# Kernel tuning notes

Hardware: AMD Instinct MI355X
Metric: run time of the kernel (lower is better)

Reference implementation:

```python
import jax, jax.numpy as jnp
import numpy as np
from jax import lax

B, L, D, N, NL, P = 4, 2048, 256, 16, 2, 200
CNN_CH = [(1, 128), (128, 256), (256, 256), (256, 256)]

def _pe(length, dim):
    pos = np.arange(length)[:, None].astype(np.float32)
    div = np.exp(np.arange(0, dim, 2).astype(np.float32) * (-np.log(10000.0) / dim))
    pe = np.zeros((length, dim), np.float32)
    pe[:, 0::2] = np.sin(pos * div)
    pe[:, 1::2] = np.cos(pos * div)
    return jnp.asarray(pe)

def _ln(x, g, b):
    m = x.mean(-1, keepdims=True)
    v = x.var(-1, keepdims=True)
    return (x - m) * lax.rsqrt(v + 1e-5) * g + b

def _ssm(u, A_log, dt_w, dt_b, B_w, C_w, Dp):
    # selective scan: h_t = a_t*h_{t-1} + b_t ; y_t = <h_t, C_t> + D*u_t
    dt = jax.nn.softplus(u @ dt_w + dt_b)                      # [B,L,d]
    A = -jnp.exp(A_log)                                        # [d,n]
    a = jnp.exp(dt[..., None] * A)                             # [B,L,d,n]
    Bu = jnp.einsum('bld,dn->bln', u, B_w)
    bv = dt[..., None] * Bu[:, :, None, :] * u[..., None]      # [B,L,d,n]
    C = jnp.einsum('bld,dn->bln', u, C_w)
    def step(h, ab):
        at, bt = ab
        h = at * h + bt
        return h, h
    _, hs = lax.scan(step, jnp.zeros_like(a[:, 0]), (jnp.moveaxis(a, 1, 0), jnp.moveaxis(bv, 1, 0)))
    hs = jnp.moveaxis(hs, 0, 1)                                # [B,L,d,n]
    return jnp.einsum('bldn,bln->bld', hs, C) + u * Dp

def _bimamba(x, g, bt, in_w, in_b, A_log, dt_w, dt_b, B_w, C_w, Dp, out_w, out_b):
    h = _ln(x, g, bt)
    u, z = jnp.split(h @ in_w + in_b, 2, axis=-1)
    u = jax.nn.silu(u)
    yf = _ssm(u, A_log[0], dt_w[0], dt_b[0], B_w[0], C_w[0], Dp[0])
    yb = jnp.flip(_ssm(jnp.flip(u, 1), A_log[1], dt_w[1], dt_b[1], B_w[1], C_w[1], Dp[1]), 1)
    return ((yf + yb) * jax.nn.silu(z)) @ out_w + out_b

def _forward(x, pairs, emb_w, emb_b, conv0_w, conv0_b, bn0_g, bn0_b, conv1_w, conv1_b, bn1_g, bn1_b, conv2_w, conv2_b, bn2_g, bn2_b, conv3_w, conv3_b, bn3_g, bn3_b, fp_w, fp_b, mb_norm_g, mb_norm_b, mb_in_w, mb_in_b, mb_A_log, mb_dt_w, mb_dt_b, mb_B_w, mb_C_w, mb_D, mb_out_w, mb_out_b, me_w1, me_b1, me_w2, me_b2, mew, ep_w, ep_b, epi_w1, epi_b1, epi_w2, epi_b2, epi_w3, epi_b3, out_w1, out_b1, out_w2, out_b2):
    x_embed = x[..., None] * emb_w + emb_b                     # snp_embedding: Linear(1,D)
    h = x[:, None, :]                                          # [B,1,L]
    for cw, cb, g, b in ((conv0_w, conv0_b, bn0_g, bn0_b), (conv1_w, conv1_b, bn1_g, bn1_b), (conv2_w, conv2_b, bn2_g, bn2_b), (conv3_w, conv3_b, bn3_g, bn3_b)):
        h = lax.conv_general_dilated(h, cw, (1,), [(1, 1)], dimension_numbers=('NCH', 'OIH', 'NCH')) + cb[None, :, None]
        h = jax.nn.relu(g[None, :, None] * h + b[None, :, None])  # eval-mode BatchNorm (running stats)
    x_cnn = jnp.transpose(h, (0, 2, 1))                        # [B,L,C]
    xm = x_embed + (x_cnn @ fp_w + fp_b) + _pe(L, D)           # combine + sinusoidal PE
    for l in range(NL):
        xm = xm + _bimamba(xm, mb_norm_g[l], mb_norm_b[l], mb_in_w[l], mb_in_b[l], mb_A_log[l], mb_dt_w[l], mb_dt_b[l], mb_B_w[l], mb_C_w[l], mb_D[l], mb_out_w[l], mb_out_b[l])
    x_final = xm
    x_main = jax.nn.relu(x @ me_w1 + me_b1) @ me_w2 + me_b2    # main_effect MLP
    main_weights = jax.nn.sigmoid(mew)
    # batched pairwise epistasis scoring (replaces the Python pair loop)
    fi = x_final[:, pairs[:, 0], :]                            # [B,P,D]
    fj = x_final[:, pairs[:, 1], :]
    scores = jax.nn.sigmoid(jnp.concatenate([fi, fj], -1) @ ep_w + ep_b)[..., 0].mean(0)  # [P]
    top_scores, top_idx = lax.top_k(scores, P)
    top_pairs = pairs[top_idx]
    x_flat = jnp.concatenate([x_cnn.mean(1), x_final.mean(1), x_main], -1)  # [B, C+D+16]
    e = jax.nn.relu(x_flat @ epi_w1 + epi_b1)
    e = jax.nn.relu(e @ epi_w2 + epi_b2)
    e = e @ epi_w3 + epi_b3
    pred = jax.nn.sigmoid(jax.nn.relu(e @ out_w1 + out_b1) @ out_w2 + out_b2)
    return pred, main_weights, top_pairs, top_scores

def setup_inputs():
    kit = iter(jax.random.split(jax.random.key(0), 64))
    def nrm(shape, s=0.02):
        return jax.random.normal(next(kit), shape, jnp.float32) * s
    z = lambda *s: jnp.zeros(s, jnp.float32)
    o = lambda *s: jnp.ones(s, jnp.float32)
    inp = {}
    inp['x'] = jax.random.normal(next(kit), (B, L), jnp.float32)
    i = jax.random.randint(next(kit), (P,), 0, L)
    off = jax.random.randint(next(kit), (P,), 1, L)
    inp['pairs'] = jnp.stack([i, (i + off) % L], axis=1).astype(jnp.int32)
    inp['emb_w'] = nrm((D,), 0.1); inp['emb_b'] = z(D)
    for li, (ci, co) in enumerate(CNN_CH):
        inp['conv%d_w' % li] = nrm((co, ci, 3), 0.1)
        inp['conv%d_b' % li] = z(co)
        inp['bn%d_g' % li] = o(co)
        inp['bn%d_b' % li] = z(co)
    inp['fp_w'] = nrm((CNN_CH[-1][1], D)); inp['fp_b'] = z(D)
    inp['mb_norm_g'] = o(NL, D); inp['mb_norm_b'] = z(NL, D)
    inp['mb_in_w'] = nrm((NL, D, 2 * D)); inp['mb_in_b'] = z(NL, 2 * D)
    inp['mb_A_log'] = jnp.log(jnp.broadcast_to(jnp.arange(1, N + 1, dtype=jnp.float32), (NL, 2, D, N)))
    inp['mb_dt_w'] = nrm((NL, 2, D, D)); inp['mb_dt_b'] = jnp.full((NL, 2, D), -3.0, jnp.float32)
    inp['mb_B_w'] = nrm((NL, 2, D, N)); inp['mb_C_w'] = nrm((NL, 2, D, N))
    inp['mb_D'] = o(NL, 2, D)
    inp['mb_out_w'] = nrm((NL, D, D)); inp['mb_out_b'] = z(NL, D)
    inp['me_w1'] = nrm((L, D)); inp['me_b1'] = z(D)
    inp['me_w2'] = nrm((D, 16)); inp['me_b2'] = z(16)
    inp['mew'] = jax.random.normal(next(kit), (L,), jnp.float32)
    inp['ep_w'] = nrm((2 * D, 1)); inp['ep_b'] = z(1)
    inp['epi_w1'] = nrm((CNN_CH[-1][1] + D + 16, 128)); inp['epi_b1'] = z(128)
    inp['epi_w2'] = nrm((128, 64)); inp['epi_b2'] = z(64)
    inp['epi_w3'] = nrm((64, 32)); inp['epi_b3'] = z(32)
    inp['out_w1'] = nrm((32, 16)); inp['out_b1'] = z(16)
    inp['out_w2'] = nrm((16, 1)); inp['out_b2'] = z(1)
    return inp

def reference(x, pairs, emb_w, emb_b, conv0_w, conv0_b, bn0_g, bn0_b, conv1_w, conv1_b, bn1_g, bn1_b, conv2_w, conv2_b, bn2_g, bn2_b, conv3_w, conv3_b, bn3_g, bn3_b, fp_w, fp_b, mb_norm_g, mb_norm_b, mb_in_w, mb_in_b, mb_A_log, mb_dt_w, mb_dt_b, mb_B_w, mb_C_w, mb_D, mb_out_w, mb_out_b, me_w1, me_b1, me_w2, me_b2, mew, ep_w, ep_b, epi_w1, epi_b1, epi_w2, epi_b2, epi_w3, epi_b3, out_w1, out_b1, out_w2, out_b2):
    return _forward(x, pairs, emb_w, emb_b, conv0_w, conv0_b, bn0_g, bn0_b, conv1_w, conv1_b, bn1_g, bn1_b, conv2_w, conv2_b, bn2_g, bn2_b, conv3_w, conv3_b, bn3_g, bn3_b, fp_w, fp_b, mb_norm_g, mb_norm_b, mb_in_w, mb_in_b, mb_A_log, mb_dt_w, mb_dt_b, mb_B_w, mb_C_w, mb_D, mb_out_w, mb_out_b, me_w1, me_b1, me_w2, me_b2, mew, ep_w, ep_b, epi_w1, epi_b1, epi_w2, epi_b2, epi_w3, epi_b3, out_w1, out_b1, out_w2, out_b2)
```

## Files before the change

### kernel.cpp

```cpp
#include <hip/hip_runtime.h>
#include <math.h>

typedef unsigned short u16;
typedef unsigned int u32;
typedef __attribute__((ext_vector_type(8))) short short8;
typedef __attribute__((ext_vector_type(4))) float f32x4;

#define BB 4
#define LSEQ 2048
static const size_t SZ = (size_t)BB * LSEQ * 256;

#define NCH 64
#define CT 32

__device__ __forceinline__ float b2f(u32 u) { return __uint_as_float(u); }

__device__ __forceinline__ void split3(float x, u16& h, u16& m, u16& l) {
    u32 xu = __float_as_uint(x);
    u32 hu = (xu + 0x7FFFu + ((xu >> 16) & 1u)) & 0xFFFF0000u;
    h = (u16)(hu >> 16);
    float r1 = x - b2f(hu);
    u32 r1u = __float_as_uint(r1);
    u32 mu = (r1u + 0x7FFFu + ((r1u >> 16) & 1u)) & 0xFFFF0000u;
    m = (u16)(mu >> 16);
    float r2 = r1 - b2f(mu);
    u32 lu = __float_as_uint(r2);
    l = (u16)((lu + 0x7FFFu + ((lu >> 16) & 1u)) >> 16);
}

__device__ __forceinline__ float rc3(const u16* __restrict__ h, const u16* __restrict__ m,
                                     const u16* __restrict__ l, size_t i) {
    return b2f((u32)h[i] << 16) + b2f((u32)m[i] << 16) + b2f((u32)l[i] << 16);
}

__global__ void wsplit_t(const float* __restrict__ W, int Kd, int Nd, int total,
                         u16* __restrict__ oh, u16* __restrict__ om, u16* __restrict__ ol) {
    int idx = blockIdx.x * 256 + threadIdx.x;
    if (idx >= total) return;
    int per = Kd * Nd;
    int mat = idx / per;
    int r = idx - mat * per;
    int n = r / Kd;
    int k = r - n * Kd;
    float v = W[(size_t)mat * per + (size_t)k * Nd + n];
    split3(v, oh[idx], om[idx], ol[idx]);
}

__global__ void wsplit_conv(const float* __restrict__ w, int CI, int total,
                            u16* __restrict__ oh, u16* __restrict__ om, u16* __restrict__ ol) {
    int idx = blockIdx.x * 256 + threadIdx.x;
    if (idx >= total) return;
    int ci = idx % CI;
    int tmp = idx / CI;
    int co = tmp & 255;
    int tap = tmp >> 8;
    float v = w[(co * CI + ci) * 3 + tap];
    split3(v, oh[idx], om[idx], ol[idx]);
}

__global__ void wsplit_bc(const float* __restrict__ Bw, const float* __restrict__ Cw,
                          u16* __restrict__ oh, u16* __restrict__ om, u16* __restrict__ ol) {
    int idx = blockIdx.x * 256 + threadIdx.x;
    int layer = idx >> 14;
    int r = idx & 16383;
    int n = r >> 8, k = r & 255;
    int dir = n >> 5, which = (n >> 4) & 1, col = n & 15;
    const float* src = which ? Cw : Bw;
    float v = src[layer * 8192 + dir * 4096 + k * 16 + col];
    split3(v, oh[idx], om[idx], ol[idx]);
}

__global__ __launch_bounds__(256) void conv0_k(const float* __restrict__ x, const float* __restrict__ w,
                                               const float* __restrict__ cb, const float* __restrict__ g,
                                               const float* __restrict__ bb, u16* __restrict__ oh,
                                               u16* __restrict__ om, u16* __restrict__ ol) {
    int gid = blockIdx.x * 256 + threadIdx.x;
    int co = gid & 127;
    int l = (gid >> 7) & (LSEQ - 1);
    int b = gid >> 18;
    const float* xr = x + (size_t)b * LSEQ;
    float xm1 = (l > 0) ? xr[l - 1] : 0.f;
    float x0 = xr[l];
    float xp1 = (l < LSEQ - 1) ? xr[l + 1] : 0.f;
    float v = xm1 * w[co * 3] + x0 * w[co * 3 + 1] + xp1 * w[co * 3 + 2] + cb[co];
    v = fmaxf(g[co] * v + bb[co], 0.f);
    size_t o = ((size_t)b * LSEQ + l) * 128 + co;
    split3(v, oh[o], om[o], ol[o]);
}

#define MODE_FP 0
#define MODE_UZ 1
#define MODE_DT 2
#define MODE_OUT 3
#define MODE_BC 4

__global__ __launch_bounds__(256, 2) void mfma_gemm_k(
    const u16* __restrict__ Ah, const u16* __restrict__ Am, const u16* __restrict__ Al,
    const u16* __restrict__ Bh_, const u16* __restrict__ Bm_, const u16* __restrict__ Bl_,
    const float* __restrict__ bias, int mode, float* __restrict__ outf,
    u16* __restrict__ oh, u16* __restrict__ om, u16* __restrict__ ol,
    const float* __restrict__ resid, const float* __restrict__ xv,
    const float* __restrict__ embw, const float* __restrict__ embb,
    int bz, int biasz, long oz) {
    __shared__ __attribute__((aligned(16))) u16 AhL[32 * 264];
    __shared__ __attribute__((aligned(16))) u16 AmL[32 * 264];
    __shared__ __attribute__((aligned(16))) u16 AlL[32 * 264];
    int t = threadIdx.x;
    int w = t >> 6, l = t & 63;
    int lo16 = l & 15, q = l >> 4;
    int zi = blockIdx.z;
    const u16* bh = Bh_ + (size_t)zi * bz;
    const u16* bm = Bm_ + (size_t)zi * bz;
    const u16* bl = Bl_ + (size_t)zi * bz;
    int ncol = blockIdx.y * 64 + w * 16 + lo16;
    short8 Brh[8], Brm[8], Brl[8];
#pragma unroll
    for (int ks = 0; ks < 8; ++ks) {
        size_t boff = (size_t)ncol * 256 + ks * 32 + q * 8;
        Brh[ks] = *(const short8*)&bh[boff];
        Brm[ks] = *(const short8*)&bm[boff];
        Brl[ks] = *(const short8*)&bl[boff];
    }
    float bv = bias ? bias[biasz * zi + ncol] : 0.f;
    int m_base = blockIdx.x * 64;
    for (int c = 0; c < 2; ++c) {
        int m0 = m_base + c * 32;
        if (c) __syncthreads();
#pragma unroll
        for (int j = 0; j < 4; ++j) {
            int idx = t + j * 256;
            int r = idx >> 5, p = idx & 31;
            size_t goff = (size_t)(m0 + r) * 256 + p * 8;
            int loff = r * 264 + p * 8;
            *(short8*)&AhL[loff] = *(const short8*)&Ah[goff];
            *(short8*)&AmL[loff] = *(const short8*)&Am[goff];
            *(short8*)&AlL[loff] = *(const short8*)&Al[goff];
        }
        __syncthreads();
        f32x4 acc0 = {0.f, 0.f, 0.f, 0.f}, acc1 = {0.f, 0.f, 0.f, 0.f};
#pragma unroll
        for (int ks = 0; ks < 8; ++ks) {
            int koff = ks * 32 + q * 8;
            short8 a0h = *(const short8*)&AhL[lo16 * 264 + koff];
            short8 a0m = *(const short8*)&AmL[lo16 * 264 + koff];
            short8 a0l = *(const short8*)&AlL[lo16 * 264 + koff];
            short8 a1h = *(const short8*)&AhL[(16 + lo16) * 264 + koff];
            short8 a1m = *(const short8*)&AmL[(16 + lo16) * 264 + koff];
            short8 a1l = *(const short8*)&AlL[(16 + lo16) * 264 + koff];
            acc0 = __builtin_amdgcn_mfma_f32_16x16x32_bf16(a0h, Brh[ks], acc0, 0, 0, 0);
            acc0 = __builtin_amdgcn_mfma_f32_16x16x32_bf16(a0h, Brm[ks], acc0, 0, 0, 0);
            acc0 = __builtin_amdgcn_mfma_f32_16x16x32_bf16(a0m, Brh[ks], acc0, 0, 0, 0);
            acc0 = __builtin_amdgcn_mfma_f32_16x16x32_bf16(a0h, Brl[ks], acc0, 0, 0, 0);
            acc0 = __builtin_amdgcn_mfma_f32_16x16x32_bf16(a0m, Brm[ks], acc0, 0, 0, 0);
            acc0 = __builtin_amdgcn_mfma_f32_16x16x32_bf16(a0l, Brh[ks], acc0, 0, 0, 0);
            acc1 = __builtin_amdgcn_mfma_f32_16x16x32_bf16(a1h, Brh[ks], acc1, 0, 0, 0);
            acc1 = __builtin_amdgcn_mfma_f32_16x16x32_bf16(a1h, Brm[ks], acc1, 0, 0, 0);
            acc1 = __builtin_amdgcn_mfma_f32_16x16x32_bf16(a1m, Brh[ks], acc1, 0, 0, 0);
            acc1 = __builtin_amdgcn_mfma_f32_16x16x32_bf16(a1h, Brl[ks], acc1, 0, 0, 0);
            acc1 = __builtin_amdgcn_mfma_f32_16x16x32_bf16(a1m, Brm[ks], acc1, 0, 0, 0);
            acc1 = __builtin_amdgcn_mfma_f32_16x16x32_bf16(a1l, Brh[ks], acc1, 0, 0, 0);
        }
        float freq = 0.f;
        if (mode == MODE_FP) freq = expf(-(float)(ncol & ~1) * (logf(10000.f) / 256.f));
#pragma unroll
        for (int mt = 0; mt < 2; ++mt) {
            f32x4 a = mt ? acc1 : acc0;
#pragma unroll
            for (int r = 0; r < 4; ++r) {
                int row = m0 + mt * 16 + q * 4 + r;
                float v = a[r] + bv;
                size_t o = (size_t)row * 256 + ncol;
                if (mode == MODE_FP) {
                    int li = row & (LSEQ - 1);
                    float ang = (float)li * freq;
                    float pe = (ncol & 1) ? cosf(ang) : sinf(ang);
                    v += xv[row] * embw[ncol] + embb[ncol] + pe;
                    outf[o] = v;
                } else if (mode == MODE_UZ) {
                    if (ncol < 256) {
                        v = v / (1.f + __expf(-v));
                        split3(v, oh[o], om[o], ol[o]);
                    } else {
                        outf[(size_t)row * 256 + ncol - 256] = v;
                    }
                } else if (mode == MODE_DT) {
                    v = (v > 20.f) ? v : log1pf(__expf(v));
                    outf[(size_t)zi * oz + o] = v;
                } else if (mode == MODE_BC) {
                    outf[(size_t)row * 64 + ncol] = v;
                } else {
                    v += resid[o];
                    outf[o] = v;
                }
            }
        }
    }
}

template <int CI, int KS>
__global__ __launch_bounds__(256, 2) void conv_mfma_k(
    const u16* __restrict__ Ah, const u16* __restrict__ Am, const u16* __restrict__ Al,
    const u16* __restrict__ Wh, const u16* __restrict__ Wm, const u16* __restrict__ Wl,
    const float* __restrict__ cb, const float* __restrict__ bg, const float* __restrict__ bb,
    u16* __restrict__ oh, u16* __restrict__ om, u16* __restrict__ ol) {
    const int STR = CI + 8;
    __shared__ __attribute__((aligned(16))) u16 AhL[34 * STR];
    __shared__ __attribute__((aligned(16))) u16 AmL[34 * STR];
    __shared__ __attribute__((aligned(16))) u16 AlL[34 * STR];
    int t = threadIdx.x, w = t >> 6, l = t & 63;
    int lo16 = l & 15, q = l >> 4;
    int ncol = blockIdx.y * 64 + w * 16 + lo16;
    int m_base = blockIdx.x * 64;
    float cbv = cb[ncol], gv = bg[ncol], bbv = bb[ncol];
    for (int c = 0; c < 2; ++c) {
        int m0 = m_base + c * 32;
        if (c) __syncthreads();
        const int PARTS = CI / 8;
        for (int idx = t; idx < 34 * PARTS; idx += 256) {
            int r = idx / PARTS, p = idx - r * PARTS;
            long goff = (long)(m0 - 1 + r) * CI + p * 8;
            int loff = r * STR + p * 8;
            *(short8*)&AhL[loff] = *(const short8*)(Ah + goff);
            *(short8*)&AmL[loff] = *(const short8*)(Am + goff);
            *(short8*)&AlL[loff] = *(const short8*)(Al + goff);
        }
        __syncthreads();
        f32x4 acc0 = {0.f, 0.f, 0.f, 0.f}, acc1 = {0.f, 0.f, 0.f, 0.f};
#pragma unroll
        for (int tap = 0; tap < 3; ++tap) {
            short8 Brh[KS], Brm[KS], Brl[KS];
#pragma unroll
            for (int ks = 0; ks < KS; ++ks) {
                size_t boff = ((size_t)(tap * 256) + ncol) * CI + ks * 32 + q * 8;
                Brh[ks] = *(const short8*)&Wh[boff];
                Brm[ks] = *(const short8*)&Wm[boff];
                Brl[ks] = *(const short8*)&Wl[boff];
            }
#pragma unroll
            for (int ks = 0; ks < KS; ++ks) {
                int koff = ks * 32 + q * 8;
                int r0 = (lo16 + tap) * STR + koff;
                int r1 = (16 + lo16 + tap) * STR + koff;
                short8 a0h = *(const short8*)&AhL[r0];
                short8 a0m = *(const short8*)&AmL[r0];
                short8 a0l = *(const short8*)&AlL[r0];
                short8 a1h = *(const short8*)&AhL[r1];
                short8 a1m = *(const short8*)&AmL[r1];
                short8 a1l = *(const short8*)&AlL[r1];
                acc0 = __builtin_amdgcn_mfma_f32_16x16x32_bf16(a0h, Brh[ks], acc0, 0, 0, 0);
                acc0 = __builtin_amdgcn_mfma_f32_16x16x32_bf16(a0h, Brm[ks], acc0, 0, 0, 0);
                acc0 = __builtin_amdgcn_mfma_f32_16x16x32_bf16(a0m, Brh[ks], acc0, 0, 0, 0);
                acc0 = __builtin_amdgcn_mfma_f32_16x16x32_bf16(a0h, Brl[ks], acc0, 0, 0, 0);
                acc0 = __builtin_amdgcn_mfma_f32_16x16x32_bf16(a0m, Brm[ks], acc0, 0, 0, 0);
                acc0 = __builtin_amdgcn_mfma_f32_16x16x32_bf16(a0l, Brh[ks], acc0, 0, 0, 0);
                acc1 = __builtin_amdgcn_mfma_f32_16x16x32_bf16(a1h, Brh[ks], acc1, 0, 0, 0);
                acc1 = __builtin_amdgcn_mfma_f32_16x16x32_bf16(a1h, Brm[ks], acc1, 0, 0, 0);
                acc1 = __builtin_amdgcn_mfma_f32_16x16x32_bf16(a1m, Brh[ks], acc1, 0, 0, 0);
                acc1 = __builtin_amdgcn_mfma_f32_16x16x32_bf16(a1h, Brl[ks], acc1, 0, 0, 0);
                acc1 = __builtin_amdgcn_mfma_f32_16x16x32_bf16(a1m, Brm[ks], acc1, 0, 0, 0);
                acc1 = __builtin_amdgcn_mfma_f32_16x16x32_bf16(a1l, Brh[ks], acc1, 0, 0, 0);
            }
        }
#pragma unroll
        for (int mt = 0; mt < 2; ++mt) {
            f32x4 a = mt ? acc1 : acc0;
#pragma unroll
            for (int r = 0; r < 4; ++r) {
                int row = m0 + mt * 16 + q * 4 + r;
                float v = fmaxf(gv * (a[r] + cbv) + bbv, 0.f);
                size_t o = (size_t)row * 256 + ncol;
                split3(v, oh[o], om[o], ol[o]);
            }
        }
    }
}

template <int CI>
__global__ __launch_bounds__(256) void convfix_k(const u16* __restrict__ inh, const u16* __restrict__ inm,
                                                 const u16* __restrict__ inl, const u16* __restrict__ wh,
                                                 const u16* __restrict__ wm, const u16* __restrict__ wl,
                                                 const float* __restrict__ cb, const float* __restrict__ bg,
                                                 const float* __restrict__ bb, u16* __restrict__ oh,
                                                 u16* __restrict__ om, u16* __restrict__ ol) {
    int b = blockIdx.x, side = blockIdx.y;
    int w = threadIdx.x >> 6, lane = threadIdx.x & 63;
    int co = blockIdx.z * 4 + w;
    int l = side ? (LSEQ - 1) : 0;
    int tap0 = side ? 0 : 1;
    float acc = 0.f;
#pragma unroll
    for (int tp = 0; tp < 2; ++tp) {
        int tap = tap0 + tp;
        int li = l + tap - 1;
        size_t ibase = ((size_t)b * LSEQ + li) * CI;
        size_t wbase = ((size_t)(tap * 256) + co) * CI;
        for (int ci = lane; ci < CI; ci += 64)
            acc += rc3(inh, inm, inl, ibase + ci) * rc3(wh, wm, wl, wbase + ci);
    }
    for (int off = 32; off; off >>= 1) acc += __shfl_xor(acc, off, 64);
    if (lane == 0) {
        float v = fmaxf(bg[co] * (acc + cb[co]) + bb[co], 0.f);
        size_t o = ((size_t)b * LSEQ + l) * 256 + co;
        split3(v, oh[o], om[o], ol[o]);
    }
}

__global__ __launch_bounds__(256) void ln_k(const float* __restrict__ xin, const float* __restrict__ g,
                                            const float* __restrict__ b, u16* __restrict__ oh,
                                            u16* __restrict__ om, u16* __restrict__ ol) {
    int t = threadIdx.x;
    int w = t >> 6, lane = t & 63;
    size_t row = (size_t)blockIdx.x * 4 + w;
    float4 v = *(const float4*)&xin[row * 256 + lane * 4];
    float s = v.x + v.y + v.z + v.w;
    float qq = v.x * v.x + v.y * v.y + v.z * v.z + v.w * v.w;
    for (int off = 32; off; off >>= 1) {
        s += __shfl_xor(s, off, 64);
        qq += __shfl_xor(qq, off, 64);
    }
    float m = s * (1.f / 256.f);
    float var = qq * (1.f / 256.f) - m * m;
    float r = rsqrtf(var + 1e-5f);
    float4 gg = *(const float4*)&g[lane * 4];
    float4 bb4 = *(const float4*)&b[lane * 4];
    float o0 = (v.x - m) * r * gg.x + bb4.x;
    float o1 = (v.y - m) * r * gg.y + bb4.y;
    float o2 = (v.z - m) * r * gg.z + bb4.z;
    float o3 = (v.w - m) * r * gg.w + bb4.w;
    u16 h[4], mm[4], ll[4];
    split3(o0, h[0], mm[0], ll[0]);
    split3(o1, h[1], mm[1], ll[1]);
    split3(o2, h[2], mm[2], ll[2]);
    split3(o3, h[3], mm[3], ll[3]);
    size_t i = row * 256 + lane * 4;
    uint2 p;
    p.x = (u32)h[0] | ((u32)h[1] << 16); p.y = (u32)h[2] | ((u32)h[3] << 16);
    *(uint2*)&oh[i] = p;
    p.x = (u32)mm[0] | ((u32)mm[1] << 16); p.y = (u32)mm[2] | ((u32)mm[3] << 16);
    *(uint2*)&om[i] = p;
    p.x = (u32)ll[0] | ((u32)ll[1] << 16); p.y = (u32)ll[2] | ((u32)ll[3] << 16);
    *(uint2*)&ol[i] = p;
}

__global__ __launch_bounds__(256) void scan1_k(const float* __restrict__ dtbuf, const u16* __restrict__ uh,
                                               const u16* __restrict__ um, const u16* __restrict__ ul,
                                               const float* __restrict__ bc, const float* __restrict__ A_log,
                                               float* __restrict__ stA, float* __restrict__ stB) {
    int c = blockIdx.x, dgq = blockIdx.y;
    int b = blockIdx.z >> 1, dir = blockIdx.z & 1;
    int t = threadIdx.x;
    int dl = t >> 2, ng = t & 3;
    int d = dgq * 64 + dl;
    float4 Alv = *(const float4*)&A_log[(dir * 256 + d) * 16 + ng * 4];
    float Ac0 = -__expf(Alv.x), Ac1 = -__expf(Alv.y), Ac2 = -__expf(Alv.z), Ac3 = -__expf(Alv.w);
    const float* dtp = dtbuf + (size_t)dir * SZ;
    __shared__ __attribute__((aligned(16))) float s_dt[CT * 68];
    __shared__ __attribute__((aligned(16))) float s_u[CT * 68];
    __shared__ __attribute__((aligned(16))) float s_bu[CT * 20];
#pragma unroll
    for (int rep = 0; rep < 2; ++rep) {
        int idx = t + rep * 256;
        int i = idx >> 4, seg = idx & 15;
        int sq = c * CT + i;
        int tt = dir ? (LSEQ - 1 - sq) : sq;
        size_t rowoff = ((size_t)b * LSEQ + tt) * 256 + dgq * 64 + seg * 4;
        *(float4*)&s_dt[i * 68 + seg * 4] = *(const float4*)&dtp[rowoff];
        uint2 hh = *(const uint2*)&uh[rowoff], mm = *(const uint2*)&um[rowoff], ll = *(const uint2*)&ul[rowoff];
        float4 vv;
        vv.x = b2f(hh.x << 16) + b2f(mm.x << 16) + b2f(ll.x << 16);
        vv.y = b2f(hh.x & 0xFFFF0000u) + b2f(mm.x & 0xFFFF0000u) + b2f(ll.x & 0xFFFF0000u);
        vv.z = b2f(hh.y << 16) + b2f(mm.y << 16) + b2f(ll.y << 16);
        vv.w = b2f(hh.y & 0xFFFF0000u) + b2f(mm.y & 0xFFFF0000u) + b2f(ll.y & 0xFFFF0000u);
        *(float4*)&s_u[i * 68 + seg * 4] = vv;
    }
    if (t < 128) {
        int i = t >> 2, seg = t & 3;
        int sq = c * CT + i;
        int tt = dir ? (LSEQ - 1 - sq) : sq;
        *(float4*)&s_bu[i * 20 + seg * 4] = *(const float4*)&bc[((size_t)b * LSEQ + tt) * 64 + dir * 32 + seg * 4];
    }
    __syncthreads();
    float h0 = 0.f, h1 = 0.f, h2 = 0.f, h3 = 0.f;
    float A0 = 1.f, A1 = 1.f, A2 = 1.f, A3 = 1.f;
#pragma unroll
    for (int i = 0; i < CT; ++i) {
        float dtv = s_dt[i * 68 + dl];
        float uv = s_u[i * 68 + dl];
        float4 bu = *(const float4*)&s_bu[i * 20 + ng * 4];
        float du = dtv * uv;
        float a0 = __expf(dtv * Ac0), a1 = __expf(dtv * Ac1), a2 = __expf(dtv * Ac2), a3 = __expf(dtv * Ac3);
        A0 *= a0; A1 *= a1; A2 *= a2; A3 *= a3;
        h0 = a0 * h0 + du * bu.x;
        h1 = a1 * h1 + du * bu.y;
        h2 = a2 * h2 + du * bu.z;
        h3 = a3 * h3 + du * bu.w;
    }
    size_t o = ((size_t)(b * 2 + dir) * NCH + c) * 4096 + dgq * 1024 + dl * 16 + ng * 4;
    float4 av = {A0, A1, A2, A3};
    float4 hv = {h0, h1, h2, h3};
    *(float4*)&stA[o] = av;
    *(float4*)&stB[o] = hv;
}

__global__ __launch_bounds__(256) void scan2_k(const float* __restrict__ stA, const float* __restrict__ stB,
                                               float* __restrict__ stH) {
    int g = blockIdx.x * 256 + threadIdx.x;
    int bd = g >> 12;
    int idx = g & 4095;
    size_t base = (size_t)bd * NCH * 4096 + idx;
    float h = 0.f;
#pragma unroll 8
    for (int c = 0; c < NCH; ++c) {
        stH[base + (size_t)c * 4096] = h;
        h = stA[base + (size_t)c * 4096] * h + stB[base + (size_t)c * 4096];
    }
}

__global__ __launch_bounds__(256) void scan3_k(const float* __restrict__ dtbuf, const u16* __restrict__ uh,
                                               const u16* __restrict__ um, const u16* __restrict__ ul,
                                               const float* __restrict__ bc, const float* __restrict__ A_log,
                                               const float* __restrict__ Dp, const float* __restrict__ stH,
                                               float* __restrict__ y0, float* __restrict__ y1) {
    int c = blockIdx.x, dgq = blockIdx.y;
    int b = blockIdx.z >> 1, dir = blockIdx.z & 1;
    int t = threadIdx.x;
// ... 176 lines not shown

__global__ __launch_bounds__(128) void epi_k(const float* __restrict__ xflat, const float* __restrict__ w1,
                                             const float* __restrict__ b1, const float* __restrict__ w2,
                                             const float* __restrict__ b2, const float* __restrict__ w3,
                                             const float* __restrict__ b3, const float* __restrict__ ow1,
                                             const float* __restrict__ ob1, const float* __restrict__ ow2,
                                             const float* __restrict__ ob2, float* __restrict__ outp) {
    int b = blockIdx.x, t = threadIdx.x;
    __shared__ float xb[528], e1[128], e2[64], e3[32], o1[16];
    for (int idx = t; idx < 528; idx += 128) xb[idx] = xflat[b * 528 + idx];
    __syncthreads();
    {
        float a = b1[t];
        for (int k = 0; k < 528; ++k) a += xb[k] * w1[k * 128 + t];
        e1[t] = fmaxf(a, 0.f);
    }
    __syncthreads();
    if (t < 64) {
        float a = b2[t];
        for (int k = 0; k < 128; ++k) a += e1[k] * w2[k * 64 + t];
        e2[t] = fmaxf(a, 0.f);
    }
    __syncthreads();
    if (t < 32) {
        float a = b3[t];
        for (int k = 0; k < 64; ++k) a += e2[k] * w3[k * 32 + t];
        e3[t] = a;
    }
    __syncthreads();
    if (t < 16) {
        float a = ob1[t];
        for (int k = 0; k < 32; ++k) a += e3[k] * ow1[k * 16 + t];
        o1[t] = fmaxf(a, 0.f);
    }
    __syncthreads();
    if (t == 0) {
        float a = ob2[0];
        for (int k = 0; k < 16; ++k) a += o1[k] * ow2[k];
        outp[b] = 1.f / (1.f + __expf(-a));
    }
}

extern "C" void kernel_launch(void* const* d_in, const int* in_sizes, int n_in, void* d_out, int out_size,
                              void* d_ws, size_t ws_size, hipStream_t stream) {
    (void)in_sizes; (void)n_in; (void)out_size; (void)ws_size;
    const float* x = (const float*)d_in[0];
    const int* pairs = (const int*)d_in[1];
    const float* emb_w = (const float*)d_in[2];
    const float* emb_b = (const float*)d_in[3];
    const float* conv0_w = (const float*)d_in[4];
    const float* conv0_b = (const float*)d_in[5];
    const float* bn0_g = (const float*)d_in[6];
    const float* bn0_b = (const float*)d_in[7];
    const float* conv1_w = (const float*)d_in[8];
    const float* conv1_b = (const float*)d_in[9];
    const float* bn1_g = (const float*)d_in[10];
    const float* bn1_b = (const float*)d_in[11];
    const float* conv2_w = (const float*)d_in[12];
    const float* conv2_b = (const float*)d_in[13];
    const float* bn2_g = (const float*)d_in[14];
    const float* bn2_b = (const float*)d_in[15];
    const float* conv3_w = (const float*)d_in[16];
    const float* conv3_b = (const float*)d_in[17];
    const float* bn3_g = (const float*)d_in[18];
    const float* bn3_b = (const float*)d_in[19];
    const float* fp_w = (const float*)d_in[20];
    const float* fp_b = (const float*)d_in[21];
    const float* mb_norm_g = (const float*)d_in[22];
    const float* mb_norm_b = (const float*)d_in[23];
    const float* mb_in_w = (const float*)d_in[24];
    const float* mb_in_b = (const float*)d_in[25];
    const float* mb_A_log = (const float*)d_in[26];
    const float* mb_dt_w = (const float*)d_in[27];
    const float* mb_dt_b = (const float*)d_in[28];
    const float* mb_B_w = (const float*)d_in[29];
    const float* mb_C_w = (const float*)d_in[30];
    const float* mb_D = (const float*)d_in[31];
    const float* mb_out_w = (const float*)d_in[32];
    const float* mb_out_b = (const float*)d_in[33];
    const float* me_w1 = (const float*)d_in[34];
    const float* me_b1 = (const float*)d_in[35];
    const float* me_w2 = (const float*)d_in[36];
    const float* me_b2 = (const float*)d_in[37];
    const float* mew = (const float*)d_in[38];
    const float* ep_w = (const float*)d_in[39];
    const float* ep_b = (const float*)d_in[40];
    const float* epi_w1 = (const float*)d_in[41];
    const float* epi_b1 = (const float*)d_in[42];
    const float* epi_w2 = (const float*)d_in[43];
    const float* epi_b2 = (const float*)d_in[44];
    const float* epi_w3 = (const float*)d_in[45];
    const float* epi_b3 = (const float*)d_in[46];
    const float* out_w1 = (const float*)d_in[47];
    const float* out_b1 = (const float*)d_in[48];
    const float* out_w2 = (const float*)d_in[49];
    const float* out_b2 = (const float*)d_in[50];
    float* outp = (float*)d_out;

    float* ws = (float*)d_ws;
    size_t off = 0;
    auto AL = [&](size_t n) { float* p = ws + off; off += n; return p; };
    float* xm = AL(SZ);
    float* z = AL(SZ);
    float* dtb = AL(2 * SZ);
    float* y0 = AL(SZ);
    float* y1 = AL(SZ);
    float* bcb = AL(SZ / 4);
    AL(128);
    float* c1s = AL(SZ + SZ / 2);
    AL(128);
    float* c2s = AL(SZ + SZ / 2);
    AL(128);
    float* c3s = AL(SZ + SZ / 2);
    AL(128);
    float* wfp = AL(98304);
    float* win = AL(393216);
    float* wdt = AL(393216);
    float* wou = AL(196608);
    float* wc1 = AL(147456);
    float* wc2 = AL(294912);
    float* wc3 = AL(294912);
    float* wbc = AL(49152);
    float* part = AL(65536);
    float* part2 = AL(16384);
    float* xflat = AL(2112);
    float* scoresb = AL(256);

    u16* c0h = (u16*)dtb + 128;
    u16* c0m = c0h + SZ / 2;
    u16* c0l = c0m + SZ / 2;
    u16* c1h = (u16*)c1s; u16* c1m = c1h + SZ; u16* c1l = c1m + SZ;
    u16* c2h = (u16*)c2s; u16* c2m = c2h + SZ; u16* c2l = c2m + SZ;
    u16* c3h = (u16*)c3s; u16* c3m = c3h + SZ; u16* c3l = c3m + SZ;
    float* stH = c1s;
    u16* wfph = (u16*)wfp; u16* wfpm = wfph + 65536; u16* wfpl = wfpm + 65536;
    u16* winh = (u16*)win; u16* winm = winh + 262144; u16* winl = winm + 262144;
    u16* wdth = (u16*)wdt; u16* wdtm = wdth + 262144; u16* wdtl = wdtm + 262144;
    u16* wouh = (u16*)wou; u16* woum = wouh + 131072; u16* woul = woum + 131072;
    u16* wc1h = (u16*)wc1; u16* wc1m = wc1h + 98304; u16* wc1l = wc1m + 98304;
    u16* wc2h = (u16*)wc2; u16* wc2m = wc2h + 196608; u16* wc2l = wc2m + 196608;
    u16* wc3h = (u16*)wc3; u16* wc3m = wc3h + 196608; u16* wc3l = wc3m + 196608;
    u16* wbch = (u16*)wbc; u16* wbcm = wbch + 32768; u16* wbcl = wbcm + 32768;

    wsplit_t<<<256, 256, 0, stream>>>(fp_w, 256, 256, 65536, wfph, wfpm, wfpl);
    wsplit_t<<<1024, 256, 0, stream>>>(mb_in_w, 256, 512, 262144, winh, winm, winl);
    wsplit_t<<<1024, 256, 0, stream>>>(mb_dt_w, 256, 256, 262144, wdth, wdtm, wdtl);
    wsplit_t<<<512, 256, 0, stream>>>(mb_out_w, 256, 256, 131072, wouh, woum, woul);
    wsplit_conv<<<384, 256, 0, stream>>>(conv1_w, 128, 98304, wc1h, wc1m, wc1l);
    wsplit_conv<<<768, 256, 0, stream>>>(conv2_w, 256, 196608, wc2h, wc2m, wc2l);
    wsplit_conv<<<768, 256, 0, stream>>>(conv3_w, 256, 196608, wc3h, wc3m, wc3l);
    wsplit_bc<<<128, 256, 0, stream>>>(mb_B_w, mb_C_w, wbch, wbcm, wbcl);

    conv0_k<<<4096, 256, 0, stream>>>(x, conv0_w, conv0_b, bn0_g, bn0_b, c0h, c0m, c0l);
    conv_mfma_k<128, 4><<<dim3(128, 4), 256, 0, stream>>>(c0h, c0m, c0l, wc1h, wc1m, wc1l, conv1_b, bn1_g, bn1_b,
                                                          c1h, c1m, c1l);
    convfix_k<128><<<dim3(4, 2, 64), 256, 0, stream>>>(c0h, c0m, c0l, wc1h, wc1m, wc1l, conv1_b, bn1_g, bn1_b,
                                                       c1h, c1m, c1l);
    conv_mfma_k<256, 8><<<dim3(128, 4), 256, 0, stream>>>(c1h, c1m, c1l, wc2h, wc2m, wc2l, conv2_b, bn2_g, bn2_b,
                                                          c2h, c2m, c2l);
    convfix_k<256><<<dim3(4, 2, 64), 256, 0, stream>>>(c1h, c1m, c1l, wc2h, wc2m, wc2l, conv2_b, bn2_g, bn2_b,
                                                       c2h, c2m, c2l);
    conv_mfma_k<256, 8><<<dim3(128, 4), 256, 0, stream>>>(c2h, c2m, c2l, wc3h, wc3m, wc3l, conv3_b, bn3_g, bn3_b,
                                                          c3h, c3m, c3l);
    convfix_k<256><<<dim3(4, 2, 64), 256, 0, stream>>>(c2h, c2m, c2l, wc3h, wc3m, wc3l, conv3_b, bn3_g, bn3_b,
                                                       c3h, c3m, c3l);

    mfma_gemm_k<<<dim3(128, 4, 1), 256, 0, stream>>>(c3h, c3m, c3l, wfph, wfpm, wfpl, fp_b, MODE_FP, xm,
                                                     nullptr, nullptr, nullptr, nullptr, x, emb_w, emb_b, 0, 0, 0);

    for (int l = 0; l < 2; ++l) {
        ln_k<<<2048, 256, 0, stream>>>(xm, mb_norm_g + l * 256, mb_norm_b + l * 256, c1h, c1m, c1l);
        mfma_gemm_k<<<dim3(128, 8, 1), 256, 0, stream>>>(c1h, c1m, c1l, winh + l * 131072, winm + l * 131072,
                                                         winl + l * 131072, mb_in_b + l * 512, MODE_UZ, z,
                                                         c2h, c2m, c2l, nullptr, nullptr, nullptr, nullptr, 0, 0, 0);
        mfma_gemm_k<<<dim3(128, 4, 2), 256, 0, stream>>>(c2h, c2m, c2l, wdth + 2 * l * 65536, wdtm + 2 * l * 65536,
                                                         wdtl + 2 * l * 65536, mb_dt_b + l * 512, MODE_DT, dtb,
                                                         nullptr, nullptr, nullptr, nullptr, nullptr, nullptr,
                                                         nullptr, 65536, 256, (long)SZ);
        mfma_gemm_k<<<dim3(128, 1, 1), 256, 0, stream>>>(c2h, c2m, c2l, wbch + l * 16384, wbcm + l * 16384,
                                                         wbcl + l * 16384, nullptr, MODE_BC, bcb,
                                                         nullptr, nullptr, nullptr, nullptr, nullptr, nullptr,
                                                         nullptr, 0, 0, 0);
        scan1_k<<<dim3(NCH, 4, 8), 256, 0, stream>>>(dtb, c2h, c2m, c2l, bcb, mb_A_log + l * 8192, y0, y1);
        scan2_k<<<128, 256, 0, stream>>>(y0, y1, stH);
        scan3_k<<<dim3(NCH, 4, 8), 256, 0, stream>>>(dtb, c2h, c2m, c2l, bcb, mb_A_log + l * 8192, mb_D + l * 512,
                                                     stH, y0, y1);
        gate_k<<<2048, 256, 0, stream>>>(y0, y1, z, c1h, c1m, c1l);
        mfma_gemm_k<<<dim3(128, 4, 1), 256, 0, stream>>>(c1h, c1m, c1l, wouh + l * 65536, woum + l * 65536,
                                                         woul + l * 65536, mb_out_b + l * 256, MODE_OUT, xm,
                                                         nullptr, nullptr, nullptr, xm, nullptr, nullptr, nullptr,
                                                         0, 0, 0);
    }

    mean1_k<<<dim3(4, 32), 256, 0, stream>>>(c3h, c3m, c3l, xm, part);
    mean2_k<<<4, 256, 0, stream>>>(part, xflat);
    xmain1_k<<<dim3(4, 16), 256, 0, stream>>>(x, me_w1, part2);
    xmain2_k<<<4, 256, 0, stream>>>(part2, me_b1, me_w2, me_b2, xflat);
    mew_k<<<8, 256, 0, stream>>>(mew, outp);
    scores_k<<<200, 256, 0, stream>>>(xm, pairs, ep_w, ep_b, scoresb);
    topk_k<<<1, 256, 0, stream>>>(scoresb, pairs, outp);
    epi_k<<<4, 128, 0, stream>>>(xflat, epi_w1, epi_b1, epi_w2, epi_b2, epi_w3, epi_b3, out_w1, out_b1, out_w2,
                                 out_b2, outp);
}
```

Baseline: 686.0 us.

## Retile MFMA GEMM and conv kernels to 16-row blocks looping over column groups

The GEMM and conv kernels now give each block 16 rows instead of 64, load the A tile into shared memory once, and loop over all column groups inside the block. Before, the grid was split along columns, with each block reloading B fragments and computing two 16-row subtiles. The aim is to reuse the A tile across every output column and cut the redundant A loads across column blocks. In exchange, B weights are now reloaded from global memory for every 16-row block, each wave has only one accumulator chain per step, and every block does serial work over the column groups.

```diff
diff --git a/kernel.cpp b/kernel.cpp
--- a/kernel.cpp
+++ b/kernel.cpp
@@ -101,10 +101,10 @@
     u16* __restrict__ oh, u16* __restrict__ om, u16* __restrict__ ol,
     const float* __restrict__ resid, const float* __restrict__ xv,
     const float* __restrict__ embw, const float* __restrict__ embb,
-    int bz, int biasz, long oz) {
-    __shared__ __attribute__((aligned(16))) u16 AhL[32 * 264];
-    __shared__ __attribute__((aligned(16))) u16 AmL[32 * 264];
-    __shared__ __attribute__((aligned(16))) u16 AlL[32 * 264];
+    int ng, int bz, int biasz, long oz) {
+    __shared__ __attribute__((aligned(16))) u16 AhL[16 * 264];
+    __shared__ __attribute__((aligned(16))) u16 AmL[16 * 264];
+    __shared__ __attribute__((aligned(16))) u16 AlL[16 * 264];
     int t = threadIdx.x;
     int w = t >> 6, l = t & 63;
     int lo16 = l & 15, q = l >> 4;
@@ -112,86 +112,71 @@
     const u16* bh = Bh_ + (size_t)zi * bz;
     const u16* bm = Bm_ + (size_t)zi * bz;
     const u16* bl = Bl_ + (size_t)zi * bz;
-    int ncol = blockIdx.y * 64 + w * 16 + lo16;
-    short8 Brh[8], Brm[8], Brl[8];
-#pragma unroll
-    for (int ks = 0; ks < 8; ++ks) {
-        size_t boff = (size_t)ncol * 256 + ks * 32 + q * 8;
-        Brh[ks] = *(const short8*)&bh[boff];
-        Brm[ks] = *(const short8*)&bm[boff];
-        Brl[ks] = *(const short8*)&bl[boff];
-    }
-    float bv = bias ? bias[biasz * zi + ncol] : 0.f;
-    int m_base = blockIdx.x * 64;
-    for (int c = 0; c < 2; ++c) {
-        int m0 = m_base + c * 32;
-        if (c) __syncthreads();
-#pragma unroll
-        for (int j = 0; j < 4; ++j) {
-            int idx = t + j * 256;
-            int r = idx >> 5, p = idx & 31;
-            size_t goff = (size_t)(m0 + r) * 256 + p * 8;
-            int loff = r * 264 + p * 8;
-            *(short8*)&AhL[loff] = *(const short8*)&Ah[goff];
-            *(short8*)&AmL[loff] = *(const short8*)&Am[goff];
-            *(short8*)&AlL[loff] = *(const short8*)&Al[goff];
+    int m0 = blockIdx.x * 16;
+#pragma unroll
+    for (int j = 0; j < 2; ++j) {
+        int idx = t + j * 256;
+        int r = idx >> 5, p = idx & 31;
+        size_t goff = (size_t)(m0 + r) * 256 + p * 8;
+        int loff = r * 264 + p * 8;
+        *(short8*)&AhL[loff] = *(const short8*)&Ah[goff];
+        *(short8*)&AmL[loff] = *(const short8*)&Am[goff];
+        *(short8*)&AlL[loff] = *(const short8*)&Al[goff];
+    }
+    __syncthreads();
+    for (int g = 0; g < ng; ++g) {
+        int ncol = g * 64 + w * 16 + lo16;
+        short8 Brh[8], Brm[8], Brl[8];
+#pragma unroll
+        for (int ks = 0; ks < 8; ++ks) {
+            size_t boff = (size_t)ncol * 256 + ks * 32 + q * 8;
+            Brh[ks] = *(const short8*)&bh[boff];
+            Brm[ks] = *(const short8*)&bm[boff];
+            Brl[ks] = *(const short8*)&bl[boff];
         }
-        __syncthreads();
-        f32x4 acc0 = {0.f, 0.f, 0.f, 0.f}, acc1 = {0.f, 0.f, 0.f, 0.f};
+        float bv = bias ? bias[biasz * zi + ncol] : 0.f;
+        f32x4 acc = {0.f, 0.f, 0.f, 0.f};
 #pragma unroll
         for (int ks = 0; ks < 8; ++ks) {
             int koff = ks * 32 + q * 8;
-            short8 a0h = *(const short8*)&AhL[lo16 * 264 + koff];
-            short8 a0m = *(const short8*)&AmL[lo16 * 264 + koff];
-            short8 a0l = *(const short8*)&AlL[lo16 * 264 + koff];
-            short8 a1h = *(const short8*)&AhL[(16 + lo16) * 264 + koff];
-            short8 a1m = *(const short8*)&AmL[(16 + lo16) * 264 + koff];
-            short8 a1l = *(const short8*)&AlL[(16 + lo16) * 264 + koff];
-            acc0 = __builtin_amdgcn_mfma_f32_16x16x32_bf16(a0h, Brh[ks], acc0, 0, 0, 0);
-            acc0 = __builtin_amdgcn_mfma_f32_16x16x32_bf16(a0h, Brm[ks], acc0, 0, 0, 0);
-            acc0 = __builtin_amdgcn_mfma_f32_16x16x32_bf16(a0m, Brh[ks], acc0, 0, 0, 0);
-            acc0 = __builtin_amdgcn_mfma_f32_16x16x32_bf16(a0h, Brl[ks], acc0, 0, 0, 0);
-            acc0 = __builtin_amdgcn_mfma_f32_16x16x32_bf16(a0m, Brm[ks], acc0, 0, 0, 0);
-            acc0 = __builtin_amdgcn_mfma_f32_16x16x32_bf16(a0l, Brh[ks], acc0, 0, 0, 0);
-            acc1 = __builtin_amdgcn_mfma_f32_16x16x32_bf16(a1h, Brh[ks], acc1, 0, 0, 0);
-            acc1 = __builtin_amdgcn_mfma_f32_16x16x32_bf16(a1h, Brm[ks], acc1, 0, 0, 0);
-            acc1 = __builtin_amdgcn_mfma_f32_16x16x32_bf16(a1m, Brh[ks], acc1, 0, 0, 0);
-            acc1 = __builtin_amdgcn_mfma_f32_16x16x32_bf16(a1h, Brl[ks], acc1, 0, 0, 0);
-            acc1 = __builtin_amdgcn_mfma_f32_16x16x32_bf16(a1m, Brm[ks], acc1, 0, 0, 0);
-            acc1 = __builtin_amdgcn_mfma_f32_16x16x32_bf16(a1l, Brh[ks], acc1, 0, 0, 0);
+            short8 ah = *(const short8*)&AhL[lo16 * 264 + koff];
+            short8 am = *(const short8*)&AmL[lo16 * 264 + koff];
+            short8 al = *(const short8*)&AlL[lo16 * 264 + koff];
+            acc = __builtin_amdgcn_mfma_f32_16x16x32_bf16(ah, Brh[ks], acc, 0, 0, 0);
+            acc = __builtin_amdgcn_mfma_f32_16x16x32_bf16(ah, Brm[ks], acc, 0, 0, 0);
+            acc = __builtin_amdgcn_mfma_f32_16x16x32_bf16(am, Brh[ks], acc, 0, 0, 0);
+            acc = __builtin_amdgcn_mfma_f32_16x16x32_bf16(ah, Brl[ks], acc, 0, 0, 0);
+            acc = __builtin_amdgcn_mfma_f32_16x16x32_bf16(am, Brm[ks], acc, 0, 0, 0);
+            acc = __builtin_amdgcn_mfma_f32_16x16x32_bf16(al, Brh[ks], acc, 0, 0, 0);
         }
         float freq = 0.f;
         if (mode == MODE_FP) freq = expf(-(float)(ncol & ~1) * (logf(10000.f) / 256.f));
 #pragma unroll
-        for (int mt = 0; mt < 2; ++mt) {
-            f32x4 a = mt ? acc1 : acc0;
-#pragma unroll
-            for (int r = 0; r < 4; ++r) {
-                int row = m0 + mt * 16 + q * 4 + r;
-                float v = a[r] + bv;
-                size_t o = (size_t)row * 256 + ncol;
-                if (mode == MODE_FP) {
-                    int li = row & (LSEQ - 1);
-                    float ang = (float)li * freq;
-                    float pe = (ncol & 1) ? cosf(ang) : sinf(ang);
-                    v += xv[row] * embw[ncol] + embb[ncol] + pe;
-                    outf[o] = v;
-                } else if (mode == MODE_UZ) {
-                    if (ncol < 256) {
-                        v = v / (1.f + __expf(-v));
-                        split3(v, oh[o], om[o], ol[o]);
-                    } else {
-                        outf[(size_t)row * 256 + ncol - 256] = v;
-                    }
-                } else if (mode == MODE_DT) {
-                    v = (v > 20.f) ? v : log1pf(__expf(v));
-                    outf[(size_t)zi * oz + o] = v;
-                } else if (mode == MODE_BC) {
-                    outf[(size_t)row * 64 + ncol] = v;
+        for (int r = 0; r < 4; ++r) {
+            int row = m0 + q * 4 + r;
+            float v = acc[r] + bv;
+            size_t o = (size_t)row * 256 + ncol;
+            if (mode == MODE_FP) {
+                int li = row & (LSEQ - 1);
+                float ang = (float)li * freq;
+                float pe = (ncol & 1) ? cosf(ang) : sinf(ang);
+                v += xv[row] * embw[ncol] + embb[ncol] + pe;
+                outf[o] = v;
+            } else if (mode == MODE_UZ) {
+                if (ncol < 256) {
+                    v = v / (1.f + __expf(-v));
+                    split3(v, oh[o], om[o], ol[o]);
                 } else {
-                    v += resid[o];
-                    outf[o] = v;
+                    outf[(size_t)row * 256 + ncol - 256] = v;
                 }
+            } else if (mode == MODE_DT) {
+                v = (v > 20.f) ? v : log1pf(__expf(v));
+                outf[(size_t)zi * oz + o] = v;
+            } else if (mode == MODE_BC) {
+                outf[(size_t)row * 64 + ncol] = v;
+            } else {
+                v += resid[o];
+                outf[o] = v;
             }
         }
     }
@@ -204,28 +189,26 @@
     const float* __restrict__ cb, const float* __restrict__ bg, const float* __restrict__ bb,
     u16* __restrict__ oh, u16* __restrict__ om, u16* __restrict__ ol) {
     const int STR = CI + 8;
-    __shared__ __attribute__((aligned(16))) u16 AhL[34 * STR];
-    __shared__ __attribute__((aligned(16))) u16 AmL[34 * STR];
-    __shared__ __attribute__((aligned(16))) u16 AlL[34 * STR];
+    __shared__ __attribute__((aligned(16))) u16 AhL[18 * STR];
+    __shared__ __attribute__((aligned(16))) u16 AmL[18 * STR];
+    __shared__ __attribute__((aligned(16))) u16 AlL[18 * STR];
     int t = threadIdx.x, w = t >> 6, l = t & 63;
     int lo16 = l & 15, q = l >> 4;
-    int ncol = blockIdx.y * 64 + w * 16 + lo16;
-    int m_base = blockIdx.x * 64;
-    float cbv = cb[ncol], gv = bg[ncol], bbv = bb[ncol];
-    for (int c = 0; c < 2; ++c) {
-        int m0 = m_base + c * 32;
-        if (c) __syncthreads();
-        const int PARTS = CI / 8;
-        for (int idx = t; idx < 34 * PARTS; idx += 256) {
-            int r = idx / PARTS, p = idx - r * PARTS;
-            long goff = (long)(m0 - 1 + r) * CI + p * 8;
-            int loff = r * STR + p * 8;
-            *(short8*)&AhL[loff] = *(const short8*)(Ah + goff);
-            *(short8*)&AmL[loff] = *(const short8*)(Am + goff);
-            *(short8*)&AlL[loff] = *(const short8*)(Al + goff);
-        }
-        __syncthreads();
-        f32x4 acc0 = {0.f, 0.f, 0.f, 0.f}, acc1 = {0.f, 0.f, 0.f, 0.f};
+    int m0 = blockIdx.x * 16;
+    const int PARTS = CI / 8;
+    for (int idx = t; idx < 18 * PARTS; idx += 256) {
+        int r = idx / PARTS, p = idx - r * PARTS;
+        long goff = (long)(m0 - 1 + r) * CI + p * 8;
+        int loff = r * STR + p * 8;
+        *(short8*)&AhL[loff] = *(const short8*)(Ah + goff);
+        *(short8*)&AmL[loff] = *(const short8*)(Am + goff);
+        *(short8*)&AlL[loff] = *(const short8*)(Al + goff);
+    }
+    __syncthreads();
+    for (int g = 0; g < 4; ++g) {
+        int ncol = g * 64 + w * 16 + lo16;
+        float cbv = cb[ncol], gv = bg[ncol], bbv = bb[ncol];
+        f32x4 acc = {0.f, 0.f, 0.f, 0.f};
 #pragma unroll
         for (int tap = 0; tap < 3; ++tap) {
             short8 Brh[KS], Brm[KS], Brl[KS];
@@ -240,37 +223,23 @@
             for (int ks = 0; ks < KS; ++ks) {
                 int koff = ks * 32 + q * 8;
                 int r0 = (lo16 + tap) * STR + koff;
-                int r1 = (16 + lo16 + tap) * STR + koff;
-                short8 a0h = *(const short8*)&AhL[r0];
-                short8 a0m = *(const short8*)&AmL[r0];
-                short8 a0l = *(const short8*)&AlL[r0];
-                short8 a1h = *(const short8*)&AhL[r1];
-                short8 a1m = *(const short8*)&AmL[r1];
-                short8 a1l = *(const short8*)&AlL[r1];
-                acc0 = __builtin_amdgcn_mfma_f32_16x16x32_bf16(a0h, Brh[ks], acc0, 0, 0, 0);
-                acc0 = __builtin_amdgcn_mfma_f32_16x16x32_bf16(a0h, Brm[ks], acc0, 0, 0, 0);
-                acc0 = __builtin_amdgcn_mfma_f32_16x16x32_bf16(a0m, Brh[ks], acc0, 0, 0, 0);
-                acc0 = __builtin_amdgcn_mfma_f32_16x16x32_bf16(a0h, Brl[ks], acc0, 0, 0, 0);
-                acc0 = __builtin_amdgcn_mfma_f32_16x16x32_bf16(a0m, Brm[ks], acc0, 0, 0, 0);
-                acc0 = __builtin_amdgcn_mfma_f32_16x16x32_bf16(a0l, Brh[ks], acc0, 0, 0, 0);
-                acc1 = __builtin_amdgcn_mfma_f32_16x16x32_bf16(a1h, Brh[ks], acc1, 0, 0, 0);
-                acc1 = __builtin_amdgcn_mfma_f32_16x16x32_bf16(a1h, Brm[ks], acc1, 0, 0, 0);
-                acc1 = __builtin_amdgcn_mfma_f32_16x16x32_bf16(a1m, Brh[ks], acc1, 0, 0, 0);
-                acc1 = __builtin_amdgcn_mfma_f32_16x16x32_bf16(a1h, Brl[ks], acc1, 0, 0, 0);
-                acc1 = __builtin_amdgcn_mfma_f32_16x16x32_bf16(a1m, Brm[ks], acc1, 0, 0, 0);
-                acc1 = __builtin_amdgcn_mfma_f32_16x16x32_bf16(a1l, Brh[ks], acc1, 0, 0, 0);
+                short8 ah = *(const short8*)&AhL[r0];
+                short8 am = *(const short8*)&AmL[r0];
+                short8 al = *(const short8*)&AlL[r0];
+                acc = __builtin_amdgcn_mfma_f32_16x16x32_bf16(ah, Brh[ks], acc, 0, 0, 0);
+                acc = __builtin_amdgcn_mfma_f32_16x16x32_bf16(ah, Brm[ks], acc, 0, 0, 0);
+                acc = __builtin_amdgcn_mfma_f32_16x16x32_bf16(am, Brh[ks], acc, 0, 0, 0);
+                acc = __builtin_amdgcn_mfma_f32_16x16x32_bf16(ah, Brl[ks], acc, 0, 0, 0);
+                acc = __builtin_amdgcn_mfma_f32_16x16x32_bf16(am, Brm[ks], acc, 0, 0, 0);
+                acc = __builtin_amdgcn_mfma_f32_16x16x32_bf16(al, Brh[ks], acc, 0, 0, 0);
             }
         }
 #pragma unroll
-        for (int mt = 0; mt < 2; ++mt) {
-            f32x4 a = mt ? acc1 : acc0;
-#pragma unroll
-            for (int r = 0; r < 4; ++r) {
-                int row = m0 + mt * 16 + q * 4 + r;
-                float v = fmaxf(gv * (a[r] + cbv) + bbv, 0.f);
-                size_t o = (size_t)row * 256 + ncol;
-                split3(v, oh[o], om[o], ol[o]);
-            }
+        for (int r = 0; r < 4; ++r) {
+            int row = m0 + q * 4 + r;
+            float v = fmaxf(gv * (acc[r] + cbv) + bbv, 0.f);
+            size_t o = (size_t)row * 256 + ncol;
+            split3(v, oh[o], om[o], ol[o]);
         }
     }
 }
@@ -753,44 +722,44 @@
     wsplit_bc<<<128, 256, 0, stream>>>(mb_B_w, mb_C_w, wbch, wbcm, wbcl);
 
     conv0_k<<<4096, 256, 0, stream>>>(x, conv0_w, conv0_b, bn0_g, bn0_b, c0h, c0m, c0l);
-    conv_mfma_k<128, 4><<<dim3(128, 4), 256, 0, stream>>>(c0h, c0m, c0l, wc1h, wc1m, wc1l, conv1_b, bn1_g, bn1_b,
-                                                          c1h, c1m, c1l);
+    conv_mfma_k<128, 4><<<512, 256, 0, stream>>>(c0h, c0m, c0l, wc1h, wc1m, wc1l, conv1_b, bn1_g, bn1_b,
+                                                 c1h, c1m, c1l);
     convfix_k<128><<<dim3(4, 2, 64), 256, 0, stream>>>(c0h, c0m, c0l, wc1h, wc1m, wc1l, conv1_b, bn1_g, bn1_b,
                                                        c1h, c1m, c1l);
-    conv_mfma_k<256, 8><<<dim3(128, 4), 256, 0, stream>>>(c1h, c1m, c1l, wc2h, wc2m, wc2l, conv2_b, bn2_g, bn2_b,
-                                                          c2h, c2m, c2l);
+    conv_mfma_k<256, 8><<<512, 256, 0, stream>>>(c1h, c1m, c1l, wc2h, wc2m, wc2l, conv2_b, bn2_g, bn2_b,
+                                                 c2h, c2m, c2l);
     convfix_k<256><<<dim3(4, 2, 64), 256, 0, stream>>>(c1h, c1m, c1l, wc2h, wc2m, wc2l, conv2_b, bn2_g, bn2_b,
                                                        c2h, c2m, c2l);
-    conv_mfma_k<256, 8><<<dim3(128, 4), 256, 0, stream>>>(c2h, c2m, c2l, wc3h, wc3m, wc3l, conv3_b, bn3_g, bn3_b,
-                                                          c3h, c3m, c3l);
+    conv_mfma_k<256, 8><<<512, 256, 0, stream>>>(c2h, c2m, c2l, wc3h, wc3m, wc3l, conv3_b, bn3_g, bn3_b,
+                                                 c3h, c3m, c3l);
     convfix_k<256><<<dim3(4, 2, 64), 256, 0, stream>>>(c2h, c2m, c2l, wc3h, wc3m, wc3l, conv3_b, bn3_g, bn3_b,
                                                        c3h, c3m, c3l);
 
-    mfma_gemm_k<<<dim3(128, 4, 1), 256, 0, stream>>>(c3h, c3m, c3l, wfph, wfpm, wfpl, fp_b, MODE_FP, xm,
-                                                     nullptr, nullptr, nullptr, nullptr, x, emb_w, emb_b, 0, 0, 0);
+    mfma_gemm_k<<<512, 256, 0, stream>>>(c3h, c3m, c3l, wfph, wfpm, wfpl, fp_b, MODE_FP, xm,
+                                         nullptr, nullptr, nullptr, nullptr, x, emb_w, emb_b, 4, 0, 0, 0);
 
     for (int l = 0; l < 2; ++l) {
         ln_k<<<2048, 256, 0, stream>>>(xm, mb_norm_g + l * 256, mb_norm_b + l * 256, c1h, c1m, c1l);
-        mfma_gemm_k<<<dim3(128, 8, 1), 256, 0, stream>>>(c1h, c1m, c1l, winh + l * 131072, winm + l * 131072,
-                                                         winl + l * 131072, mb_in_b + l * 512, MODE_UZ, z,
-                                                         c2h, c2m, c2l, nullptr, nullptr, nullptr, nullptr, 0, 0, 0);
-        mfma_gemm_k<<<dim3(128, 4, 2), 256, 0, stream>>>(c2h, c2m, c2l, wdth + 2 * l * 65536, wdtm + 2 * l * 65536,
+        mfma_gemm_k<<<512, 256, 0, stream>>>(c1h, c1m, c1l, winh + l * 131072, winm + l * 131072,
+                                             winl + l * 131072, mb_in_b + l * 512, MODE_UZ, z,
+                                             c2h, c2m, c2l, nullptr, nullptr, nullptr, nullptr, 8, 0, 0, 0);
+        mfma_gemm_k<<<dim3(512, 1, 2), 256, 0, stream>>>(c2h, c2m, c2l, wdth + 2 * l * 65536, wdtm + 2 * l * 65536,
                                                          wdtl + 2 * l * 65536, mb_dt_b + l * 512, MODE_DT, dtb,
                                                          nullptr, nullptr, nullptr, nullptr, nullptr, nullptr,
-                                                         nullptr, 65536, 256, (long)SZ);
-        mfma_gemm_k<<<dim3(128, 1, 1), 256, 0, stream>>>(c2h, c2m, c2l, wbch + l * 16384, wbcm + l * 16384,
-                                                         wbcl + l * 16384, nullptr, MODE_BC, bcb,
-                                                         nullptr, nullptr, nullptr, nullptr, nullptr, nullptr,
-                                                         nullptr, 0, 0, 0);
+                                                         nullptr, 4, 65536, 256, (long)SZ);
+        mfma_gemm_k<<<512, 256, 0, stream>>>(c2h, c2m, c2l, wbch + l * 16384, wbcm + l * 16384,
+                                             wbcl + l * 16384, nullptr, MODE_BC, bcb,
+                                             nullptr, nullptr, nullptr, nullptr, nullptr, nullptr,
+                                             nullptr, 1, 0, 0, 0);
         scan1_k<<<dim3(NCH, 4, 8), 256, 0, stream>>>(dtb, c2h, c2m, c2l, bcb, mb_A_log + l * 8192, y0, y1);
         scan2_k<<<128, 256, 0, stream>>>(y0, y1, stH);
         scan3_k<<<dim3(NCH, 4, 8), 256, 0, stream>>>(dtb, c2h, c2m, c2l, bcb, mb_A_log + l * 8192, mb_D + l * 512,
                                                      stH, y0, y1);
         gate_k<<<2048, 256, 0, stream>>>(y0, y1, z, c1h, c1m, c1l);
-        mfma_gemm_k<<<dim3(128, 4, 1), 256, 0, stream>>>(c1h, c1m, c1l, wouh + l * 65536, woum + l * 65536,
-                                                         woul + l * 65536, mb_out_b + l * 256, MODE_OUT, xm,
-                                                         nullptr, nullptr, nullptr, xm, nullptr, nullptr, nullptr,
-                                                         0, 0, 0);
+        mfma_gemm_k<<<512, 256, 0, stream>>>(c1h, c1m, c1l, wouh + l * 65536, woum + l * 65536,
+                                             woul + l * 65536, mb_out_b + l * 256, MODE_OUT, xm,
+                                             nullptr, nullptr, nullptr, xm, nullptr, nullptr, nullptr,
+                                             4, 0, 0, 0);
     }
 
     mean1_k<<<dim3(4, 32), 256, 0, stream>>>(c3h, c3m, c3l, xm, part);
```

Measured after the change: 943.6 us. +37.6%, slower.
